# Kernel optimization log

Hardware: AMD Instinct MI355X
Metric: run time of the kernel (lower is better)

## Reference

```python
import jax, jax.numpy as jnp
import numpy as np

M = 8        # number of input features
NMF = 4      # membership functions per feature
R = NMF ** M # 65536 rules
N = 1024     # batch size


def setup_inputs() -> dict:
    key = jax.random.key(0)
    k1, k2, k3, k4, k5 = jax.random.split(key, 5)
    x = jax.random.normal(k1, (N, M), dtype=jnp.float32)
    # Antecedent parameters: torch.rand -> uniform [0,1)
    center = jax.random.uniform(k2, (M, NMF), dtype=jnp.float32)
    sigma = jax.random.uniform(k3, (M, NMF), dtype=jnp.float32)
    # Consequent linear layer, init_Consequent uses uniform [0,1)
    W = jax.random.uniform(k4, (R, M), dtype=jnp.float32)
    b = jax.random.uniform(k5, (R,), dtype=jnp.float32)
    return {"x": x, "center": center, "sigma": sigma, "W": W, "b": b}


def reference(x, center, sigma, W, b):
    # droprule=False (deterministic reference; the torch drop_rule is random Bernoulli masking)
    n = x.shape[0]
    # Gaussian membership, faithful to torch: exp(-(x - c)^2 / 2 * sigma^2)
    # mg: [N, M, NMF]
    mg = jnp.exp(-((x[:, :, None] - center[None, :, :]) ** 2) * 0.5 * (sigma[None, :, :] ** 2))
    # Combinatorial rule product via mixed-radix broadcasting:
    # fg[n, r] = prod_m mg[n, m, digit_m(r)], feature 0 most significant.
    fg = mg[:, 0, :]  # [N, NMF]
    for m in range(1, M):
        fg = (fg[:, :, None] * mg[:, m, None, :]).reshape(n, -1)
    # fg: [N, R]
    fg_bar = fg / jnp.sum(fg, axis=1, keepdims=True)
    rule_out = x @ W.T + b  # [N, R]
    return jnp.sum(fg_bar * rule_out, axis=1)  # [N]
```

## Files before the change

kernel.cpp:

```cpp
#include <hip/hip_runtime.h>
#include <hip/hip_bf16.h>

typedef __attribute__((ext_vector_type(8))) short short8;
typedef __attribute__((ext_vector_type(4))) float f32x4;

#define KB 16

__device__ __forceinline__ ushort f2bf(float f) {
    __hip_bfloat16 h = __float2bfloat16(f);
    return *reinterpret_cast<ushort*>(&h);
}
__device__ __forceinline__ unsigned pk2(float a, float b) {
    return (unsigned)f2bf(a) | ((unsigned)f2bf(b) << 16);
}

__global__ __launch_bounds__(256) void fz_main(
    const float* __restrict__ x, const float* __restrict__ center,
    const float* __restrict__ sigma, const float* __restrict__ W,
    const float* __restrict__ b, float* __restrict__ out, int N)
{
    __shared__ float  xs[16][9];
    __shared__ float  mgs[16][33];
    __shared__ float  pr[16][20] __attribute__((aligned(16)));
    __shared__ ushort plf[8][64][8] __attribute__((aligned(16)));
    __shared__ float  phs[16][17];
    __shared__ float  red[4][16][9];

    const int t = threadIdx.x;
    const int tile = blockIdx.x >> 4;
    const int kb = blockIdx.x & (KB - 1);

    if (t < 128) {
        int s = t >> 3, m = t & 7;
        xs[s][m] = x[(size_t)(tile * 16 + s) * 8 + m];
    }
    __syncthreads();
    #pragma unroll
    for (int v = 0; v < 2; ++v) {
        int id = t + v * 256;
        int s = id >> 5, i = id & 31, m = i >> 2;
        float d = xs[s][m] - center[i];
        float sg = sigma[i];
        mgs[s][i] = __expf(-d * d * 0.5f * sg * sg);
    }
    __syncthreads();
    {
        int s = t >> 4, a = t & 15;
        pr[s][a] = mgs[s][24 + (a >> 2)] * mgs[s][28 + (a & 3)];
        int hi = kb * KB + a;
        phs[s][a] = mgs[s][hi >> 6] * mgs[s][4 + ((hi >> 4) & 3)]
                  * mgs[s][8 + ((hi >> 2) & 3)] * mgs[s][12 + (hi & 3)];
    }
    __syncthreads();
    {
        const int ls = t >> 5;
        #pragma unroll
        for (int oct = 0; oct < 2; ++oct) {
            const int lane_e = (2 * t + oct) & 63;
            const int s = lane_e & 15;
            const int hi3 = lane_e >> 4;
            const int L0 = ls * 32 + hi3 * 8;
            const float pqv = mgs[s][16 + (L0 >> 6)] * mgs[s][20 + ((L0 >> 4) & 3)];
            const int b7 = L0 & 8;
            const float4 r0 = *reinterpret_cast<const float4*>(&pr[s][b7]);
            const float4 r1 = *reinterpret_cast<const float4*>(&pr[s][b7 + 4]);
            unsigned Pk[4] = { pk2(pqv * r0.x, pqv * r0.y), pk2(pqv * r0.z, pqv * r0.w),
                               pk2(pqv * r1.x, pqv * r1.y), pk2(pqv * r1.z, pqv * r1.w) };
            *reinterpret_cast<short8*>(&plf[ls][lane_e][0]) =
                *reinterpret_cast<short8*>(&Pk[0]);
        }
    }
    __syncthreads();

    const int wv = t >> 6, lane = t & 63;
    const int c = lane & 15, kb4 = lane >> 4;
    short8 A[8];
    #pragma unroll
    for (int ls = 0; ls < 8; ++ls)
        A[ls] = *reinterpret_cast<const short8*>(&plf[ls][lane][0]);

    const float* src = (c < 8) ? (W + c) : b;
    const int stride = (c < 8) ? 8 : 1;
    const unsigned lmask = (c <= 8) ? 0xFFFFFFFFu : 0u;

    const int hi_base = kb * KB + wv * 4;
    const float* p = src + (size_t)(hi_base * 256 + kb4 * 8) * stride;
    const ptrdiff_t s32 = (ptrdiff_t)32 * stride;

    float bufA[8], bufB[8];
    #pragma unroll
    for (int j = 0; j < 8; ++j) bufA[j] = p[j * stride];

    f32x4 master = {0.f, 0.f, 0.f, 0.f};
    f32x4 d = {0.f, 0.f, 0.f, 0.f};
    #pragma unroll
    for (int step = 0; step < 32; ++step) {
        const float* pn = p + s32;
        float* nxt = (step & 1) ? bufA : bufB;
        if (step < 31) {
            #pragma unroll
            for (int j = 0; j < 8; ++j) nxt[j] = pn[j * stride];
        }
        const float* cu = (step & 1) ? bufB : bufA;
        unsigned Bp[4] = { pk2(cu[0], cu[1]) & lmask, pk2(cu[2], cu[3]) & lmask,
                           pk2(cu[4], cu[5]) & lmask, pk2(cu[6], cu[7]) & lmask };
        short8 B = *reinterpret_cast<short8*>(&Bp[0]);
        d = __builtin_amdgcn_mfma_f32_16x16x32_bf16(A[step & 7], B, d, 0, 0, 0);
        if ((step & 7) == 7) {
            const int hil = step >> 3;
            #pragma unroll
            for (int r = 0; r < 4; ++r)
                master[r] += phs[kb4 * 4 + r][wv * 4 + hil] * d[r];
            d = (f32x4){0.f, 0.f, 0.f, 0.f};
        }
        p = pn;
    }

    if (c < 9) {
        #pragma unroll
        for (int r = 0; r < 4; ++r)
            red[wv][kb4 * 4 + r][c] = master[r];
    }
    __syncthreads();
    if (t < 144) {
        int s = t / 9, cc = t % 9;
        red[0][s][cc] += red[1][s][cc] + red[2][s][cc] + red[3][s][cc];
    }
    __syncthreads();
    if (t < 16) {
        const int s = t;
        float denom = 1.f;
        #pragma unroll
        for (int m = 0; m < 8; ++m)
            denom *= (mgs[s][4 * m] + mgs[s][4 * m + 1] +
                      mgs[s][4 * m + 2] + mgs[s][4 * m + 3]);
        float num = red[0][s][8];
        #pragma unroll
        for (int m = 0; m < 8; ++m) num += xs[s][m] * red[0][s][m];
        atomicAdd(&out[tile * 16 + s], num / denom);
    }
}

extern "C" void kernel_launch(void* const* d_in, const int* in_sizes, int n_in,
                              void* d_out, int out_size, void* d_ws, size_t ws_size,
                              hipStream_t stream)
{
    const float* x      = (const float*)d_in[0];
    const float* center = (const float*)d_in[1];
    const float* sigma  = (const float*)d_in[2];
    const float* W      = (const float*)d_in[3];
    const float* b      = (const float*)d_in[4];
    float* out = (float*)d_out;
    const int N = in_sizes[0] / 8;

    hipMemsetAsync(out, 0, (size_t)out_size * sizeof(float), stream);
    fz_main<<<(N / 16) * KB, 256, 0, stream>>>(x, center, sigma, W, b, out, N);
}
```

Measured before the change: 77.85 us.

## Stage W and b through double-buffered LDS with coalesced loads, split K across waves

Replaces the per-lane strided global loads of W and b with coalesced float4 loads by the whole block, converted to bf16 and written into a double-buffered LDS staging area in MFMA B layout. Each wave now handles a quarter of the K dimension (two MFMAs per hi step) across all 16 hi values, instead of a quarter of the hi range over the full K. The phs table is transposed so the per-step scale is read as one float4. This is meant to cut uncoalesced global traffic and wasted lanes. In exchange it adds a block-wide barrier on every iteration and scattered 2-byte LDS stores.

```diff
diff --git a/kernel.cpp b/kernel.cpp
--- a/kernel.cpp
+++ b/kernel.cpp
@@ -23,8 +23,9 @@
     __shared__ float  mgs[16][33];
     __shared__ float  pr[16][20] __attribute__((aligned(16)));
     __shared__ ushort plf[8][64][8] __attribute__((aligned(16)));
-    __shared__ float  phs[16][17];
+    __shared__ float  phs[KB][20] __attribute__((aligned(16)));
     __shared__ float  red[4][16][9];
+    __shared__ ushort wstg[2][32][16][8] __attribute__((aligned(16)));
 
     const int t = threadIdx.x;
     const int tile = blockIdx.x >> 4;
@@ -47,9 +48,12 @@
     {
         int s = t >> 4, a = t & 15;
         pr[s][a] = mgs[s][24 + (a >> 2)] * mgs[s][28 + (a & 3)];
-        int hi = kb * KB + a;
-        phs[s][a] = mgs[s][hi >> 6] * mgs[s][4 + ((hi >> 4) & 3)]
-                  * mgs[s][8 + ((hi >> 2) & 3)] * mgs[s][12 + (hi & 3)];
+    }
+    {
+        int hil = t >> 4, s = t & 15;
+        int hi = kb * KB + hil;
+        phs[hil][s] = mgs[s][hi >> 6] * mgs[s][4 + ((hi >> 4) & 3)]
+                    * mgs[s][8 + ((hi >> 2) & 3)] * mgs[s][12 + (hi & 3)];
     }
     __syncthreads();
     {
@@ -70,50 +74,49 @@
                 *reinterpret_cast<short8*>(&Pk[0]);
         }
     }
-    __syncthreads();
 
     const int wv = t >> 6, lane = t & 63;
     const int c = lane & 15, kb4 = lane >> 4;
-    short8 A[8];
-    #pragma unroll
-    for (int ls = 0; ls < 8; ++ls)
-        A[ls] = *reinterpret_cast<const short8*>(&plf[ls][lane][0]);
+    const int srow = t >> 1, shalf = (t & 1) * 4;
 
-    const float* src = (c < 8) ? (W + c) : b;
-    const int stride = (c < 8) ? 8 : 1;
-    const unsigned lmask = (c <= 8) ? 0xFFFFFFFFu : 0u;
+    auto stage_load = [&](int hil, float4& va, float4& vb, float& bv) {
+        const float* wp = W + (size_t)(kb * KB + hil) * 2048;
+        va = *reinterpret_cast<const float4*>(wp + t * 4);
+        vb = *reinterpret_cast<const float4*>(wp + 1024 + t * 4);
+        bv = b[(kb * KB + hil) * 256 + t];
+    };
+    auto stage_write = [&](int bf, const float4& va, const float4& vb, float bv) {
+        ushort* p0 = &wstg[bf][srow >> 3][shalf][srow & 7];
+        p0[0] = f2bf(va.x); p0[8] = f2bf(va.y); p0[16] = f2bf(va.z); p0[24] = f2bf(va.w);
+        ushort* p1 = &wstg[bf][16 + (srow >> 3)][shalf][srow & 7];
+        p1[0] = f2bf(vb.x); p1[8] = f2bf(vb.y); p1[16] = f2bf(vb.z); p1[24] = f2bf(vb.w);
+        wstg[bf][t >> 3][8][t & 7] = f2bf(bv);
+    };
 
-    const int hi_base = kb * KB + wv * 4;
-    const float* p = src + (size_t)(hi_base * 256 + kb4 * 8) * stride;
-    const ptrdiff_t s32 = (ptrdiff_t)32 * stride;
+    __syncthreads();
+    short8 A0 = *reinterpret_cast<const short8*>(&plf[2 * wv][lane][0]);
+    short8 A1 = *reinterpret_cast<const short8*>(&plf[2 * wv + 1][lane][0]);
 
-    float bufA[8], bufB[8];
-    #pragma unroll
-    for (int j = 0; j < 8; ++j) bufA[j] = p[j * stride];
+    float4 va, vb2; float bv;
+    stage_load(0, va, vb2, bv);
+    stage_write(0, va, vb2, bv);
+    __syncthreads();
 
     f32x4 master = {0.f, 0.f, 0.f, 0.f};
-    f32x4 d = {0.f, 0.f, 0.f, 0.f};
-    #pragma unroll
-    for (int step = 0; step < 32; ++step) {
-        const float* pn = p + s32;
-        float* nxt = (step & 1) ? bufA : bufB;
-        if (step < 31) {
-            #pragma unroll
-            for (int j = 0; j < 8; ++j) nxt[j] = pn[j * stride];
-        }
-        const float* cu = (step & 1) ? bufB : bufA;
-        unsigned Bp[4] = { pk2(cu[0], cu[1]) & lmask, pk2(cu[2], cu[3]) & lmask,
-                           pk2(cu[4], cu[5]) & lmask, pk2(cu[6], cu[7]) & lmask };
-        short8 B = *reinterpret_cast<short8*>(&Bp[0]);
-        d = __builtin_amdgcn_mfma_f32_16x16x32_bf16(A[step & 7], B, d, 0, 0, 0);
-        if ((step & 7) == 7) {
-            const int hil = step >> 3;
-            #pragma unroll
-            for (int r = 0; r < 4; ++r)
-                master[r] += phs[kb4 * 4 + r][wv * 4 + hil] * d[r];
-            d = (f32x4){0.f, 0.f, 0.f, 0.f};
-        }
-        p = pn;
+    #pragma unroll 2
+    for (int hil = 0; hil < KB; ++hil) {
+        const int bf = hil & 1;
+        if (hil + 1 < KB) stage_load(hil + 1, va, vb2, bv);
+        f32x4 d = {0.f, 0.f, 0.f, 0.f};
+        short8 B0 = *reinterpret_cast<const short8*>(&wstg[bf][(2 * wv) * 4 + kb4][c][0]);
+        short8 B1 = *reinterpret_cast<const short8*>(&wstg[bf][(2 * wv + 1) * 4 + kb4][c][0]);
+        d = __builtin_amdgcn_mfma_f32_16x16x32_bf16(A0, B0, d, 0, 0, 0);
+        d = __builtin_amdgcn_mfma_f32_16x16x32_bf16(A1, B1, d, 0, 0, 0);
+        const float4 phv = *reinterpret_cast<const float4*>(&phs[hil][kb4 * 4]);
+        master[0] += phv.x * d[0]; master[1] += phv.y * d[1];
+        master[2] += phv.z * d[2]; master[3] += phv.w * d[3];
+        if (hil + 1 < KB) stage_write(bf ^ 1, va, vb2, bv);
+        __syncthreads();
     }
 
     if (c < 9) {
```

After: 74.27 us. 4.6% less time.
